# Kernel optimization log

Hardware: AMD Instinct MI355X
Metric: run time of the kernel (lower is better)

## Reference

```python
import jax, jax.numpy as jnp
import numpy as np

N = 50000      # nodes
E = 600000     # edges (before self loops)
F_IN = 128     # num_features
HID = 64       # num_hidden (per-head out channels of conv1)
HEADS = 8
NCLS = 16      # num_classes
NC = 16        # n_components (k_ricci feature dim)
NCP = 16       # n_components_p (e_poinc feature dim)


def _glorot(key, shape):
    lim = float(np.sqrt(6.0 / (shape[0] + shape[1])))
    return jax.random.uniform(key, shape, jnp.float32, -lim, lim)


def setup_inputs() -> dict:
    key = jax.random.key(0)
    ks = jax.random.split(key, 16)
    H1 = HEADS * HID  # 512
    return {
        "x": jax.random.normal(ks[0], (N, F_IN), jnp.float32),
        "edge_index": jax.random.randint(ks[1], (2, E), 0, N, jnp.int32),
        "alpha": jnp.ones((), jnp.float32),  # alpha_hp scalar
        "k_ricci": jax.random.normal(ks[2], (E + N, NC), jnp.float32),
        "e_poinc": jax.random.normal(ks[3], (N, NCP), jnp.float32),
        # conv1 params
        "W_src1": _glorot(ks[4], (F_IN, H1)),
        "h1_w1": _glorot(ks[5], (NC, HID)),
        "h1_w2": _glorot(ks[6], (HID, HID)),
        "h1_b2": jnp.zeros((HID,), jnp.float32),
        "p1_w1": _glorot(ks[7], (NCP, H1)),
        "p1_w2": _glorot(ks[8], (H1, H1)),
        "p1_b2": jnp.zeros((H1,), jnp.float32),
        "bias1": jnp.zeros((H1,), jnp.float32),
        # conv2 params (heads=1, concat=False)
        "W_src2": _glorot(ks[9], (H1, NCLS)),
        "h2_w1": _glorot(ks[10], (NC, NCLS)),
        "h2_w2": _glorot(ks[11], (NCLS, NCLS)),
        "h2_b2": jnp.zeros((NCLS,), jnp.float32),
        "p2_w1": _glorot(ks[12], (NCP, NCLS)),
        "p2_w2": _glorot(ks[13], (NCLS, NCLS)),
        "p2_b2": jnp.zeros((NCLS,), jnp.float32),
        "bias2": jnp.zeros((NCLS,), jnp.float32),
    }


def _segment_softmax(logits, seg, n):
    # PyG-style softmax over variable-sized segments, per channel.
    m = jax.ops.segment_max(logits, seg, num_segments=n)
    e = jnp.exp(logits - m[seg])
    s = jax.ops.segment_sum(e, seg, num_segments=n)
    return e / (s[seg] + 1e-16)


def _gat_layer(x, src, dst, k_ricci, e_poinc, alpha_hp,
               W_src, hw1, hw2, hb2, pw1, pw2, pb2, bias, H, C, concat):
    n = x.shape[0]
    xh = (x @ W_src).reshape(n, H, C)                                   # [N,H,C]
    # hmpnn MLP on per-edge Ricci features, then segment-softmax over SOURCE node
    edge_w = jax.nn.leaky_relu(k_ricci @ hw1, 0.2) @ hw2 + hb2          # [E',C]
    a = _segment_softmax(edge_w, src, n)                                # [E',C]
    msg = a[:, None, :] * xh[src]                                       # [E',H,C]
    agg = jax.ops.segment_sum(msg, dst, num_segments=n)                 # [N,H,C]
    out = agg.reshape(n, H * C) if concat else agg.mean(axis=1)
    out = out + bias
    # ham MLP on per-node Poincare features (+ extra leaky_relu, slope 0.01)
    p = jax.nn.leaky_relu(jax.nn.leaky_relu(e_poinc @ pw1, 0.2) @ pw2 + pb2, 0.01)
    return out + alpha_hp * p


def reference(x, edge_index, alpha, k_ricci, e_poinc,
              W_src1, h1_w1, h1_w2, h1_b2, p1_w1, p1_w2, p1_b2, bias1,
              W_src2, h2_w1, h2_w2, h2_b2, p2_w1, p2_w2, p2_b2, bias2):
    n = x.shape[0]
    loops = jnp.arange(n, dtype=edge_index.dtype)
    src = jnp.concatenate([edge_index[0], loops])   # add_self_loops
    dst = jnp.concatenate([edge_index[1], loops])
    h = _gat_layer(x, src, dst, k_ricci, e_poinc, alpha,
                   W_src1, h1_w1, h1_w2, h1_b2, p1_w1, p1_w2, p1_b2, bias1,
                   HEADS, HID, True)
    h = jax.nn.relu(h)
    o = _gat_layer(h, src, dst, k_ricci, e_poinc, alpha,
                   W_src2, h2_w1, h2_w2, h2_b2, p2_w1, p2_w2, p2_b2, bias2,
                   1, NCLS, False)
    return jax.nn.log_softmax(o, axis=1)
```

## Files before the change

kernel.cpp:

```cpp
#include <hip/hip_runtime.h>
#include <math.h>

#define N_NODES 50000
#define M_PAD   50048
#define N_EDGES 600000
#define E_TOT   650000
#define F_IN    128
#define HID     64
#define HEADS   8
#define H1      512
#define NCLS    16
#define NC      16
#define NCP     16
#define NBLK    ((N_NODES + 255) / 256)
#define FRNG    (N_NODES / 8)
#define FBPR    128
#define FPER    ((E_TOT + FBPR - 1) / FBPR)

typedef unsigned short u16;
typedef unsigned char  u8;
typedef __attribute__((ext_vector_type(8))) short short8;
typedef __attribute__((ext_vector_type(4))) float f32x4;
typedef __attribute__((ext_vector_type(2))) float f32x2;

__device__ __forceinline__ float bf2f(u16 h) {
    return __uint_as_float(((unsigned)h) << 16);
}
__device__ __forceinline__ u16 f2bf(float f) {
    unsigned u = __float_as_uint(f);
    u += 0x7fffu + ((u >> 16) & 1u);
    return (u16)(u >> 16);
}
__device__ __forceinline__ int edge_src(const int* __restrict__ ei, int e) {
    return (e < N_EDGES) ? ei[e] : (e - N_EDGES);
}
__device__ __forceinline__ int edge_dst(const int* __restrict__ ei, int e) {
    return (e < N_EDGES) ? ei[N_EDGES + e] : (e - N_EDGES);
}

__device__ __forceinline__ void gload16(const void* g, void* l) {
    __builtin_amdgcn_global_load_lds(
        (const __attribute__((address_space(1))) unsigned int*)g,
        (__attribute__((address_space(3))) unsigned int*)l, 16, 0, 0);
}

__global__ __launch_bounds__(256) void count_k(const int* __restrict__ ei,
                                               int* __restrict__ src_cnt, int* __restrict__ dst_cnt) {
    int e = blockIdx.x * 256 + threadIdx.x;
    if (e >= E_TOT) return;
    atomicAdd(&src_cnt[edge_src(ei, e)], 1);
    atomicAdd(&dst_cnt[edge_dst(ei, e)], 1);
}

__global__ __launch_bounds__(256) void scanA_k(const int* __restrict__ src_cnt,
                                               const int* __restrict__ dst_cnt,
                                               int* __restrict__ partials) {
    int pass = blockIdx.x >= NBLK;
    int b = blockIdx.x - pass * NBLK;
    const int* cnt = pass ? dst_cnt : src_cnt;
    int idx = b * 256 + threadIdx.x;
    int v = (idx < N_NODES) ? cnt[idx] : 0;
    __shared__ int red[4];
    #pragma unroll
    for (int off = 32; off; off >>= 1) v += __shfl_down(v, off, 64);
    if ((threadIdx.x & 63) == 0) red[threadIdx.x >> 6] = v;
    __syncthreads();
    if (threadIdx.x == 0) partials[blockIdx.x] = red[0] + red[1] + red[2] + red[3];
}

__global__ __launch_bounds__(512) void scanB_k(int* __restrict__ partials) {
    __shared__ int lds[512];
    int t = threadIdx.x;
    int seg = t >> 8, i = t & 255;
    int v = (i < NBLK) ? partials[seg * NBLK + i] : 0;
    lds[t] = v;
    __syncthreads();
    for (int d = 1; d < 256; d <<= 1) {
        int x = (i >= d) ? lds[seg * 256 + i - d] : 0;
        __syncthreads();
        lds[t] += x;
        __syncthreads();
    }
    if (i < NBLK) partials[seg * NBLK + i] = lds[t] - v;
}

__global__ __launch_bounds__(256) void scanC_k(const int* __restrict__ src_cnt,
                                               const int* __restrict__ dst_cnt,
                                               const int* __restrict__ partials,
                                               int* __restrict__ src_off, int* __restrict__ dst_off) {
    int pass = blockIdx.x >= NBLK;
    int b = blockIdx.x - pass * NBLK;
    const int* cnt = pass ? dst_cnt : src_cnt;
    int* off = pass ? dst_off : src_off;
    int base = partials[blockIdx.x];
    __shared__ int lds[256];
    int t = threadIdx.x;
    int idx = b * 256 + t;
    int v = (idx < N_NODES) ? cnt[idx] : 0;
    lds[t] = v;
    __syncthreads();
    for (int d = 1; d < 256; d <<= 1) {
        int x = (t >= d) ? lds[t - d] : 0;
        __syncthreads();
        lds[t] += x;
        __syncthreads();
    }
    if (idx < N_NODES) off[idx] = base + lds[t] - v;
    if (b == 0 && t == 0) off[N_NODES] = E_TOT;
}

__global__ __launch_bounds__(256) void fillD_k(const int* __restrict__ ei,
                                               const int* __restrict__ dst_off, int* __restrict__ dst_cur,
                                               int* __restrict__ deid, int* __restrict__ dsrc) {
    const int range = blockIdx.x & 7, slice = blockIdx.x >> 3;
    const int d0 = range * FRNG, d1 = d0 + FRNG;
    const int e0 = slice * FPER;
    const int e1 = (e0 + FPER < E_TOT) ? e0 + FPER : E_TOT;
    for (int e = e0 + threadIdx.x; e < e1; e += 256) {
        int d = edge_dst(ei, e);
        if (d < d0 || d >= d1) continue;
        int rd = dst_off[d] + atomicAdd(&dst_cur[d], 1);
        deid[rd] = e;
        dsrc[rd] = edge_src(ei, e);
    }
}

__global__ __launch_bounds__(256) void fillS_k(const int* __restrict__ dsrc,
                                               const int* __restrict__ src_off, int* __restrict__ src_cur,
                                               int* __restrict__ src_list) {
    const int range = blockIdx.x & 7, slice = blockIdx.x >> 3;
    const int s0 = range * FRNG, s1 = s0 + FRNG;
    const int r0 = slice * FPER;
    const int r1 = (r0 + FPER < E_TOT) ? r0 + FPER : E_TOT;
    for (int rd = r0 + threadIdx.x; rd < r1; rd += 256) {
        int s = dsrc[rd];
        if (s < s0 || s >= s1) continue;
        src_list[src_off[s] + atomicAdd(&src_cur[s], 1)] = rd;
    }
}

__global__ __launch_bounds__(256) void conv_a_k(const float* __restrict__ A, u16* __restrict__ Ap,
                                                int M, int Mp, int K) {
    int i = blockIdx.x * 256 + threadIdx.x;
    int total = (K >> 3) * Mp;
    if (i >= total) return;
    int r = i % Mp;
    int kb = i / Mp;
    u16* o = Ap + (size_t)i * 8;
    u16 tmp[8];
    if (r < M) {
        const float* a = A + (size_t)r * K + kb * 8;
        #pragma unroll
        for (int j = 0; j < 8; ++j) tmp[j] = f2bf(a[j]);
    } else {
        #pragma unroll
        for (int j = 0; j < 8; ++j) tmp[j] = 0;
    }
    *(ushort4*)o = *(ushort4*)tmp;
    *(ushort4*)(o + 4) = *(ushort4*)(tmp + 4);
}

__global__ __launch_bounds__(256) void conv_b_k(const float* __restrict__ B, u16* __restrict__ Bp,
                                                int K, int N) {
    int i = blockIdx.x * 256 + threadIdx.x;
    int total = (K >> 3) * N;
    if (i >= total) return;
    int n = i % N;
    int kb = i / N;
    u16 tmp[8];
    #pragma unroll
    for (int j = 0; j < 8; ++j) tmp[j] = f2bf(B[(size_t)(kb * 8 + j) * N + n]);
    u16* o = Bp + (size_t)i * 8;
    *(ushort4*)o = *(ushort4*)tmp;
    *(ushort4*)(o + 4) = *(ushort4*)(tmp + 4);
}

__device__ __forceinline__ void wfrag_one(const float* W, u16* o, int i, int K, int N) {
    int j = i & 7, lane = (i >> 3) & 63, rest = i >> 9;
    int nt = rest % (N / 16), ks = rest / (N / 16);
    int lm = lane & 15, quad = lane >> 4;
    int k = ks * 32 + quad * 8 + j, n = nt * 16 + lm;
    o[i] = (k < K) ? f2bf(W[(size_t)k * N + n]) : (u16)0;
}
__device__ __forceinline__ void wfrag_res(const float* W, u16* o, int i, int K, int N) {
    int j = i & 7, lane = (i >> 3) & 63, rest = i >> 9;
    int nt = rest % (N / 16), ks = rest / (N / 16);
    int lm = lane & 15, quad = lane >> 4;
    int k = ks * 32 + quad * 8 + j, n = nt * 16 + lm;
    float w = (k < K) ? W[(size_t)k * N + n] : 0.f;
    o[i] = f2bf(w - bf2f(f2bf(w)));
}
__global__ __launch_bounds__(256) void wfrag_all_k(
    const float* __restrict__ h1w1, const float* __restrict__ h1w2,
    const float* __restrict__ h2w1, const float* __restrict__ h2w2,
    const float* __restrict__ W2,
    u16* __restrict__ w1f, u16* __restrict__ w2f,
    u16* __restrict__ w3f, u16* __restrict__ w4f,
    u16* __restrict__ w2hf, u16* __restrict__ w2lf) {
    int i = blockIdx.x * 256 + threadIdx.x;
    if (i < 2048)       wfrag_one(h1w1, w1f, i, 16, 64);
    else if (i < 6144)  wfrag_one(h1w2, w2f, i - 2048, 64, 64);
    else if (i < 6656)  wfrag_one(h2w1, w3f, i - 6144, 16, 16);
    else if (i < 7168)  wfrag_one(h2w2, w4f, i - 6656, 16, 16);
    else if (i < 15360) wfrag_one(W2, w2hf, i - 7168, 512, 16);
    else if (i < 23552) wfrag_res(W2, w2lf, i - 15360, 512, 16);
}

template<int EPI>
__global__ __launch_bounds__(256) void mfma_gemm_k(
    const u16* __restrict__ Ap, const u16* __restrict__ Bp, u16* __restrict__ C,
    int M, int Mp, int Nn, int K,
    const float* __restrict__ bias, const u16* __restrict__ extra,
    const float* __restrict__ bias2, const float* __restrict__ alpha_p,
    const u16* __restrict__ w2hf, const u16* __restrict__ w2lf,
    float* __restrict__ xh2p)
{
    __shared__ __align__(16) char LSD[49152];
    const int t = threadIdx.x;
    const int wave = t >> 6, lane = t & 63;
    const int wm = (wave >> 1) * 64, wn = (wave & 1) * 64;
    const int lm = lane & 15, quad = lane >> 4;

    const int nwg = (int)(gridDim.y << 2);
    const int bid = (int)(blockIdx.y * 4 + blockIdx.x);
    const int qq = nwg >> 3, rr8 = nwg & 7;
    const int xcd = bid & 7, idx = bid >> 3;
    const int wg = (xcd < rr8 ? xcd * (qq + 1) : rr8 * (qq + 1) + (xcd - rr8) * qq) + idx;
    const int bn = (wg & 3) * 128;
    const int bm = (wg >> 2) * 128;

    const char* Ab = (const char*)Ap;
    const char* Bb = (const char*)Bp;

    f32x4 acc[4][4] = {};
    const int NT = K >> 5;

    auto stage = [&](int b, int ts) {
        const int kb0 = ts * 4;
        #pragma unroll
        for (int h = 0; h < 2; ++h) {
            const int ob = h * 4096 + wave * 1024;
            const int kb = kb0 + (ob >> 11);
            const int rem = (ob & 1024) + lane * 16;
            gload16(Ab + ((size_t)kb * Mp + bm) * 16 + rem, LSD + b * 8192 + ob);
            gload16(Bb + ((size_t)kb * Nn + bn) * 16 + rem, LSD + 24576 + b * 8192 + ob);
        }
    };
    auto compute = [&](int cb) {
        const u16* As = (const u16*)(LSD + cb * 8192);
        const u16* Bs = (const u16*)(LSD + 24576 + cb * 8192);
        short8 af[4], bfv[4];
        #pragma unroll
        for (int mi = 0; mi < 4; ++mi)
            af[mi] = *(const short8*)(As + quad * 1024 + (wm + mi * 16 + lm) * 8);
        #pragma unroll
        for (int nj = 0; nj < 4; ++nj)
            bfv[nj] = *(const short8*)(Bs + quad * 1024 + (wn + nj * 16 + lm) * 8);
        #pragma unroll
        for (int mi = 0; mi < 4; ++mi)
            #pragma unroll
            for (int nj = 0; nj < 4; ++nj)
                acc[mi][nj] = __builtin_amdgcn_mfma_f32_16x16x32_bf16(af[mi], bfv[nj], acc[mi][nj], 0, 0, 0);
    };

    stage(0, 0);
    stage(1, 1);
    #pragma unroll 1
    for (int ts = 0; ts < NT - 1; ++ts) {
        asm volatile("s_waitcnt vmcnt(4)" ::: "memory");
        __builtin_amdgcn_sched_barrier(0);
        __builtin_amdgcn_s_barrier();
        if (ts + 2 < NT) stage((ts + 2) % 3, ts + 2);
        compute(ts % 3);
    }
    asm volatile("s_waitcnt vmcnt(0)" ::: "memory");
    __builtin_amdgcn_sched_barrier(0);
    __builtin_amdgcn_s_barrier();
    compute((NT - 1) % 3);
    __syncthreads();

    float* Tf = (float*)LSD;
    const float alpha = (EPI == 0) ? 0.f : *alpha_p;
    short8 w2h[4], w2l[4];
    if (EPI != 0) {
        const int ksb = bn >> 5;
        #pragma unroll
        for (int kc = 0; kc < 4; ++kc) {
            w2h[kc] = *(const short8*)(w2hf + ((size_t)(ksb + kc) * 64 + lane) * 8);
            w2l[kc] = *(const short8*)(w2lf + ((size_t)(ksb + kc) * 64 + lane) * 8);
        }
    }
    #pragma unroll
    for (int pass = 0; pass < 2; ++pass) {
        if ((wave >> 1) == pass) {
            #pragma unroll
            for (int mi = 0; mi < 4; ++mi)
                #pragma unroll
                for (int r4 = 0; r4 < 4; ++r4) {
                    const int lr = mi * 16 + quad * 4 + r4;
                    const int sw = (lr & 7) << 2;
                    #pragma unroll
                    for (int nj = 0; nj < 4; ++nj)
                        Tf[lr * 128 + ((wn + nj * 16 + lm) ^ sw)] = acc[mi][nj][r4];
                }
        }
        __syncthreads();
        if (EPI == 0) {
            const int lrow = t & 63, chunk = t >> 6;
            const int col0 = chunk * 32;
            const int rr = bm + pass * 64 + lrow;
            if (rr < M) {
                const int sw = (lrow & 7) << 2;
                float v[32];
                #pragma unroll
                for (int j4 = 0; j4 < 8; ++j4) {
                    float4 f = *(const float4*)&Tf[lrow * 128 + ((col0 + j4 * 4) ^ sw)];
                    v[j4 * 4] = f.x; v[j4 * 4 + 1] = f.y; v[j4 * 4 + 2] = f.z; v[j4 * 4 + 3] = f.w;
                }
                const int gc0 = bn + col0;
                u16 pk[32];
                #pragma unroll
                for (int j = 0; j < 32; ++j) pk[j] = f2bf(v[j]);
                #pragma unroll
                for (int g = 0; g < 4; ++g)
                    *(short8*)(C + (size_t)rr * Nn + gc0 + g * 8) = *(const short8*)&pk[g * 8];
            }
        } else {
            u16* Hs = (u16*)(LSD + 32768);
            const int row = wave * 16 + lm;
            const int col0 = quad * 32;
            const int rr = bm + pass * 64 + row;
            const int gc0 = bn + col0;
            u16 hpk[32];
            if (rr < M) {
                const int sw = (row & 7) << 2;
                const u16* ex = extra + (size_t)rr * Nn + gc0;
                #pragma unroll
                for (int g = 0; g < 4; ++g) {
                    float4 f0 = *(const float4*)&Tf[row * 128 + ((col0 + g * 8) ^ sw)];
                    float4 f1 = *(const float4*)&Tf[row * 128 + ((col0 + g * 8 + 4) ^ sw)];
                    float vv8[8] = {f0.x, f0.y, f0.z, f0.w, f1.x, f1.y, f1.z, f1.w};
                    short8 e8 = *(const short8*)(ex + g * 8);
                    #pragma unroll
                    for (int j = 0; j < 8; ++j) {
                        const int cj = g * 8 + j;
                        float vv = vv8[j] + bias[gc0 + cj];
                        vv = vv > 0.f ? vv : 0.01f * vv;
                        float o = bf2f((u16)e8[j]) + bias2[gc0 + cj] + alpha * vv;
                        o = fmaxf(o, 0.f);
                        hpk[cj] = f2bf(o);
                    }
                }
            } else {
                #pragma unroll
                for (int j = 0; j < 32; ++j) hpk[j] = 0;
            }
            #pragma unroll
            for (int g = 0; g < 4; ++g) {
                const int ba = (row * 256 + quad * 64 + g * 16) ^ ((row & 7) << 4);
                *(short8*)((char*)Hs + ba) = *(const short8*)&hpk[g * 8];
            }
            __syncthreads();
            f32x4 axh = {};
            #pragma unroll
            for (int kc = 0; kc < 4; ++kc) {
                const int ba = (row * 256 + kc * 64 + quad * 16) ^ ((row & 7) << 4);
                short8 ha = *(const short8*)((const char*)Hs + ba);
                axh = __builtin_amdgcn_mfma_f32_16x16x32_bf16(ha, w2h[kc], axh, 0, 0, 0);
                axh = __builtin_amdgcn_mfma_f32_16x16x32_bf16(ha, w2l[kc], axh, 0, 0, 0);
            }
            #pragma unroll
            for (int r = 0; r < 4; ++r) {
                const int prow = bm + pass * 64 + wave * 16 + quad * 4 + r;
                if (prow < M)
                    xh2p[((size_t)(bn >> 7) * M_PAD + prow) * 16 + lm] = axh[r];
            }
        }
        __syncthreads();
    }
}

__global__ __launch_bounds__(256) void red4_k(const float* __restrict__ xh2p,
                                              float* __restrict__ xh2) {
    int i = blockIdx.x * 256 + threadIdx.x;
    if (i >= N_NODES * 4) return;
    const float4* P = (const float4*)xh2p;
    const size_t S = (size_t)M_PAD * 4;
    float4 a = P[i], b = P[S + i], c = P[2 * S + i], d = P[3 * S + i];
    float4 r;
    r.x = (a.x + b.x) + (c.x + d.x);
    r.y = (a.y + b.y) + (c.y + d.y);
    r.z = (a.z + b.z) + (c.z + d.z);
    r.w = (a.w + b.w) + (c.w + d.w);
    ((float4*)xh2)[i] = r;
}

__global__ __launch_bounds__(256) void gemm_t1_k(
    const float* __restrict__ ep, const float* __restrict__ W, u16* __restrict__ t1p)
{
    __shared__ float Bs[16][64];
    const int bm = blockIdx.y * 64, bn = blockIdx.x * 64;
    const int t = threadIdx.x;
    const int tx = t & 15, ty = t >> 4;
    *(float4*)&Bs[t >> 4][(t & 15) * 4] = *(const float4*)&W[(size_t)(t >> 4) * H1 + bn + (t & 15) * 4];
    __syncthreads();
    const int r0 = bm + ty * 4;
    const int c0 = bn + tx * 4;
    for (int i = 0; i < 4; ++i) {
        int r = r0 + i;
        if (r >= N_NODES) continue;
        float av[16];
        #pragma unroll
        for (int j4 = 0; j4 < 16; j4 += 4) {
            float4 v = *(const float4*)(ep + (size_t)r * NCP + j4);
            av[j4] = v.x; av[j4 + 1] = v.y; av[j4 + 2] = v.z; av[j4 + 3] = v.w;
        }
        u16 pk[4];
        #pragma unroll
        for (int q = 0; q < 4; ++q) {
            float s = 0.f;
            #pragma unroll
            for (int k = 0; k < 16; ++k) s = fmaf(av[k], Bs[k][tx * 4 + q], s);
            s = s > 0.f ? s : 0.2f * s;
            pk[q] = f2bf(s);
        }
        u16* o = t1p + ((size_t)(c0 >> 3) * M_PAD + r) * 8 + (c0 & 7);
        *(ushort4*)o = *(ushort4*)pk;
    }
}

#define TSTR 72
__global__ __launch_bounds__(256) void edge_mlps_k(
    const float* __restrict__ kr, const int* __restrict__ deid,
    const u16* __restrict__ w1f, const u16* __restrict__ w2f, const float* __restrict__ b2a,
    const u16* __restrict__ w3f, const u16* __restrict__ w4f, const float* __restrict__ b2b,
    u16* __restrict__ ebd, u16* __restrict__ ebd2)
{
    __shared__ __align__(16) u16 T[4][16 * TSTR];
    const int t = threadIdx.x, wv = t >> 6, lane = t & 63;
    const int lm = lane & 15, quad = lane >> 4;
    const int tile = blockIdx.x * 4 + wv;
    const int s0 = tile * 16;
    if (s0 >= E_TOT) return;
    u16* Tw = T[wv];

    short8 W1[4], W2[2][4];
    #pragma unroll
    for (int nt = 0; nt < 4; ++nt) W1[nt] = *(const short8*)(w1f + ((size_t)nt * 64 + lane) * 8);
    #pragma unroll
    for (int ks = 0; ks < 2; ++ks)
        #pragma unroll
        for (int nt = 0; nt < 4; ++nt)
            W2[ks][nt] = *(const short8*)(w2f + (((size_t)ks * 4 + nt) * 64 + lane) * 8);
    short8 W3 = *(const short8*)(w3f + (size_t)lane * 8);
    short8 W4 = *(const short8*)(w4f + (size_t)lane * 8);
    float b2av[4];
    #pragma unroll
    for (int nt = 0; nt < 4; ++nt) b2av[nt] = b2a[nt * 16 + lm];
    float b2bv = b2b[lm];

    const int e = deid[s0 + lm];
    short8 af = {};
    if (quad < 2) {
        const float* kp = kr + (size_t)e * NC + quad * 8;
        float4 v0 = *(const float4*)kp;
        float4 v1 = *(const float4*)(kp + 4);
        u16 tmp[8] = {f2bf(v0.x), f2bf(v0.y), f2bf(v0.z), f2bf(v0.w),
                      f2bf(v1.x), f2bf(v1.y), f2bf(v1.z), f2bf(v1.w)};
        af = *(const short8*)tmp;
    }

    f32x4 a1[4] = {};
    #pragma unroll
    for (int nt = 0; nt < 4; ++nt)
        a1[nt] = __builtin_amdgcn_mfma_f32_16x16x32_bf16(af, W1[nt], a1[nt], 0, 0, 0);
    #pragma unroll
    for (int nt = 0; nt < 4; ++nt)
        #pragma unroll
        for (int r = 0; r < 4; ++r) {
            float v = a1[nt][r];
            v = v > 0.f ? v : 0.2f * v;
            Tw[(quad * 4 + r) * TSTR + nt * 16 + lm] = f2bf(v);
        }
    __builtin_amdgcn_s_waitcnt(0);

    short8 a2[2];
    #pragma unroll
    for (int ks = 0; ks < 2; ++ks)
        a2[ks] = *(const short8*)&Tw[lm * TSTR + ks * 32 + quad * 8];
    f32x4 c2[4] = {};
    #pragma unroll
    for (int nt = 0; nt < 4; ++nt)
        #pragma unroll
        for (int ks = 0; ks < 2; ++ks)
            c2[nt] = __builtin_amdgcn_mfma_f32_16x16x32_bf16(a2[ks], W2[ks][nt], c2[nt], 0, 0, 0);
    #pragma unroll
    for (int nt = 0; nt < 4; ++nt)
        #pragma unroll
        for (int r = 0; r < 4; ++r)
            Tw[(quad * 4 + r) * TSTR + nt * 16 + lm] = f2bf(__expf(c2[nt][r] + b2av[nt]));
    __builtin_amdgcn_s_waitcnt(0);
    #pragma unroll
    for (int p = 0; p < 2; ++p) {
        int c = p * 64 + lane;
        int row = c >> 3, off = (c & 7) * 8;
        short8 v = *(const short8*)&Tw[row * TSTR + off];
        *(short8*)(ebd + (size_t)(s0 + row) * HID + off) = v;
    }

    f32x4 b1 = __builtin_amdgcn_mfma_f32_16x16x32_bf16(af, W3, (f32x4){}, 0, 0, 0);
    __builtin_amdgcn_s_waitcnt(0);
    #pragma unroll
    for (int r = 0; r < 4; ++r) {
        float v = b1[r];
        v = v > 0.f ? v : 0.2f * v;
        Tw[(quad * 4 + r) * TSTR + lm] = f2bf(v);
    }
    __builtin_amdgcn_s_waitcnt(0);
    short8 a3 = *(const short8*)&Tw[lm * TSTR + quad * 8];
    f32x4 c3 = __builtin_amdgcn_mfma_f32_16x16x32_bf16(a3, W4, (f32x4){}, 0, 0, 0);
    #pragma unroll
    for (int r = 0; r < 4; ++r)
        Tw[(quad * 4 + r) * TSTR + lm] = f2bf(__expf(c3[r] + b2bv));
    __builtin_amdgcn_s_waitcnt(0);
    if (lane < 32) {
        int row = lane >> 1, off = (lane & 1) * 8;
        short8 v = *(const short8*)&Tw[row * TSTR + off];
        *(short8*)(ebd2 + (size_t)(s0 + row) * NCLS + off) = v;
    }
}

__global__ __launch_bounds__(256) void s1inv_k(
    const u16* __restrict__ ebd, const int* __restrict__ src_off, const int* __restrict__ src_list,
    u16* __restrict__ xb)
{
    __shared__ float sinv[4][64];
    int gid = blockIdx.x * 256 + threadIdx.x;
    int wid = gid >> 6, lane = gid & 63, wv = threadIdx.x >> 6;
    if (wid >= N_NODES) return;
    int o0 = src_off[wid], o1 = src_off[wid + 1];
    float s0 = 0.f, s1 = 0.f, s2 = 0.f, s3 = 0.f;
    int i = o0;
    for (; i + 3 < o1; i += 4) {
        int l0 = src_list[i], l1 = src_list[i + 1], l2 = src_list[i + 2], l3 = src_list[i + 3];
        s0 += bf2f(ebd[(size_t)l0 * HID + lane]);
        s1 += bf2f(ebd[(size_t)l1 * HID + lane]);
        s2 += bf2f(ebd[(size_t)l2 * HID + lane]);
        s3 += bf2f(ebd[(size_t)l3 * HID + lane]);
    }
    for (; i < o1; ++i) {
        int sl = src_list[i];
        s0 += bf2f(ebd[(size_t)sl * HID + lane]);
    }
    sinv[wv][lane] = 1.f / (((s0 + s1) + (s2 + s3)) + 1e-16f);
    __builtin_amdgcn_s_waitcnt(0);

    const u16* xr = xb + (size_t)wid * H1 + lane * 8;
    short8 x8 = *(const short8*)xr;
    float y[8];
    #pragma unroll
    for (int j = 0; j < 8; ++j)
        y[j] = bf2f((u16)x8[j]) * sinv[wv][(lane * 8 + j) & 63];
    int p0 = 0, p1 = 0;
    p0 = __builtin_amdgcn_cvt_pk_fp8_f32(y[0], y[1], p0, false);
    p0 = __builtin_amdgcn_cvt_pk_fp8_f32(y[2], y[3], p0, true);
    p1 = __builtin_amdgcn_cvt_pk_fp8_f32(y[4], y[5], p1, false);
    p1 = __builtin_amdgcn_cvt_pk_fp8_f32(y[6], y[7], p1, true);
    uint2 pk; pk.x = (unsigned)p0; pk.y = (unsigned)p1;
    *(uint2*)((u8*)xb + (size_t)wid * (H1 * 2) + lane * 8) = pk;
}

__global__ __launch_bounds__(256) void msg1_k(
    const u16* __restrict__ ebd, const u8* __restrict__ xq,
    const int* __restrict__ dsrc, const int* __restrict__ dst_off,
    u16* __restrict__ aggb)
{
    int gid = blockIdx.x * 256 + threadIdx.x;
    int wid = gid >> 6, lane = gid & 63;
    if (wid >= N_NODES) return;
    int o0 = dst_off[wid], o1 = dst_off[wid + 1];
    const int a_off = (lane & 7) * 8;
    float acc[8] = {};
    int i = o0;
    for (; i + 3 < o1; i += 4) {
        int s0 = __builtin_nontemporal_load(dsrc + i);
        int s1 = __builtin_nontemporal_load(dsrc + i + 1);
        int s2 = __builtin_nontemporal_load(dsrc + i + 2);
        int s3 = __builtin_nontemporal_load(dsrc + i + 3);
        short8 a0 = __builtin_nontemporal_load((const short8*)(ebd + (size_t)i * HID + a_off));
        short8 a1 = __builtin_nontemporal_load((const short8*)(ebd + (size_t)(i + 1) * HID + a_off));
        short8 a2 = __builtin_nontemporal_load((const short8*)(ebd + (size_t)(i + 2) * HID + a_off));
        short8 a3 = __builtin_nontemporal_load((const short8*)(ebd + (size_t)(i + 3) * HID + a_off));
        uint2 q0 = *(const uint2*)(xq + (size_t)s0 * 1024 + lane * 8);
        uint2 q1 = *(const uint2*)(xq + (size_t)s1 * 1024 + lane * 8);
        uint2 q2 = *(const uint2*)(xq + (size_t)s2 * 1024 + lane * 8);
        uint2 q3 = *(const uint2*)(xq + (size_t)s3 * 1024 + lane * 8);
        const uint2 qs[4] = {q0, q1, q2, q3};
        const short8 as[4] = {a0, a1, a2, a3};
        #pragma unroll
        for (int u = 0; u < 4; ++u) {
            f32x2 d0 = __builtin_amdgcn_cvt_pk_f32_fp8((int)qs[u].x, false);
            f32x2 d1 = __builtin_amdgcn_cvt_pk_f32_fp8((int)qs[u].x, true);
            f32x2 d2 = __builtin_amdgcn_cvt_pk_f32_fp8((int)qs[u].y, false);
            f32x2 d3 = __builtin_amdgcn_cvt_pk_f32_fp8((int)qs[u].y, true);
            float xv[8] = {d0.x, d0.y, d1.x, d1.y, d2.x, d2.y, d3.x, d3.y};
            #pragma unroll
            for (int j = 0; j < 8; ++j)
                acc[j] = fmaf(bf2f((u16)as[u][j]), xv[j], acc[j]);
        }
    }
    for (; i < o1; ++i) {
        int s = __builtin_nontemporal_load(dsrc + i);
        short8 a8 = __builtin_nontemporal_load((const short8*)(ebd + (size_t)i * HID + a_off));
        uint2 q = *(const uint2*)(xq + (size_t)s * 1024 + lane * 8);
        f32x2 d0 = __builtin_amdgcn_cvt_pk_f32_fp8((int)q.x, false);
        f32x2 d1 = __builtin_amdgcn_cvt_pk_f32_fp8((int)q.x, true);
        f32x2 d2 = __builtin_amdgcn_cvt_pk_f32_fp8((int)q.y, false);
        f32x2 d3 = __builtin_amdgcn_cvt_pk_f32_fp8((int)q.y, true);
        float xv[8] = {d0.x, d0.y, d1.x, d1.y, d2.x, d2.y, d3.x, d3.y};
        #pragma unroll
        for (int j = 0; j < 8; ++j)
            acc[j] = fmaf(bf2f((u16)a8[j]), xv[j], acc[j]);
    }
    u16 pk[8];
    #pragma unroll
    for (int j = 0; j < 8; ++j) pk[j] = f2bf(acc[j]);
    __builtin_nontemporal_store(*(const short8*)pk, (short8*)(aggb + (size_t)wid * H1 + lane * 8));
}

__global__ __launch_bounds__(256) void s2sum_k(
    const u16* __restrict__ ebd2, const int* __restrict__ src_off, const int* __restrict__ src_list,
    float* __restrict__ inv2)
{
    int t = threadIdx.x;
    int g = blockIdx.x * 16 + (t >> 4), c = t & 15;
    if (g >= N_NODES) return;
    int o0 = src_off[g], o1 = src_off[g + 1];
    float sum = 0.f;
    for (int i = o0; i < o1; ++i) {
        int sl = src_list[i];
        sum += bf2f(ebd2[(size_t)sl * NCLS + c]);
    }
    inv2[(size_t)g * NCLS + c] = 1.f / (sum + 1e-16f);
}

__global__ __launch_bounds__(256) void msg2_k(
    const u16* __restrict__ ebd2, const float* __restrict__ inv2,
    const float* __restrict__ xh2, const int* __restrict__ dsrc,
    const int* __restrict__ dst_off, float* __restrict__ agg2)
{
    int t = threadIdx.x;
    int g = blockIdx.x * 16 + (t >> 4), c = t & 15;
    if (g >= N_NODES) return;
    int o0 = dst_off[g], o1 = dst_off[g + 1];
    float acc = 0.f;
    for (int i = o0; i < o1; ++i) {
        int s = dsrc[i];
        float a = bf2f(ebd2[(size_t)i * NCLS + c]) * inv2[(size_t)s * NCLS + c];
        acc = fmaf(a, xh2[(size_t)s * NCLS + c], acc);
    }
    agg2[(size_t)g * NCLS + c] = acc;
}

__global__ __launch_bounds__(256) void final_k(
    const float* __restrict__ agg2, const float* __restrict__ ep,
    const float* __restrict__ pw1, const float* __restrict__ pw2,
    const float* __restrict__ pb2, const float* __restrict__ bias,
    const float* __restrict__ alpha_p, float* __restrict__ out)
{
    __shared__ float s1w[256], s2w[256], sb[16], sbias[16];
    const int t = threadIdx.x;
    s1w[t] = pw1[t];
    s2w[t] = pw2[t];
    if (t < 16) { sb[t] = pb2[t]; sbias[t] = bias[t]; }
    __syncthreads();
    const int v = blockIdx.x * 256 + t;
    if (v >= N_NODES) return;
    float alpha = *alpha_p;
    float e_[16];
    #pragma unroll
    for (int j4 = 0; j4 < 16; j4 += 4) {
        float4 vv = *(const float4*)(ep + (size_t)v * 16 + j4);
        e_[j4] = vv.x; e_[j4 + 1] = vv.y; e_[j4 + 2] = vv.z; e_[j4 + 3] = vv.w;
    }
    float t2[16];
    #pragma unroll
    for (int c = 0; c < 16; ++c) {
        float s = 0.f;
        #pragma unroll
        for (int j = 0; j < 16; ++j) s = fmaf(e_[j], s1w[j * 16 + c], s);
        t2[c] = s > 0.f ? s : 0.2f * s;
    }
    float o[16];
    #pragma unroll
    for (int c4 = 0; c4 < 16; c4 += 4) {
        float4 ag = *(const float4*)(agg2 + (size_t)v * 16 + c4);
        float agv[4] = {ag.x, ag.y, ag.z, ag.w};
        #pragma unroll
        for (int q = 0; q < 4; ++q) {
            int c = c4 + q;
            float p = sb[c];
            #pragma unroll
            for (int j = 0; j < 16; ++j) p = fmaf(t2[j], s2w[j * 16 + c], p);
            p = p > 0.f ? p : 0.01f * p;
            o[c] = agv[q] + sbias[c] + alpha * p;
        }
    }
    float mx = o[0];
    #pragma unroll
    for (int c = 1; c < 16; ++c) mx = fmaxf(mx, o[c]);
    float se = 0.f;
    #pragma unroll
    for (int c = 0; c < 16; ++c) se += expf(o[c] - mx);
    float lse = mx + logf(se);
    #pragma unroll
    for (int c4 = 0; c4 < 16; c4 += 4)
        *(float4*)(out + (size_t)v * 16 + c4) =
            make_float4(o[c4] - lse, o[c4 + 1] - lse, o[c4 + 2] - lse, o[c4 + 3] - lse);
}

extern "C" void kernel_launch(void* const* d_in, const int* in_sizes, int n_in,
                              void* d_out, int out_size, void* d_ws, size_t ws_size,
                              hipStream_t stream) {
    const float* x    = (const float*)d_in[0];
    const int*   ei   = (const int*)d_in[1];
    const float* alpha= (const float*)d_in[2];
    const float* kr   = (const float*)d_in[3];
    const float* ep   = (const float*)d_in[4];
    const float* W1   = (const float*)d_in[5];
    const float* h1w1 = (const float*)d_in[6];
    const float* h1w2 = (const float*)d_in[7];
    const float* h1b2 = (const float*)d_in[8];
    const float* p1w1 = (const float*)d_in[9];
    const float* p1w2 = (const float*)d_in[10];
    const float* p1b2 = (const float*)d_in[11];
    const float* b1   = (const float*)d_in[12];
    const float* W2   = (const float*)d_in[13];
    const float* h2w1 = (const float*)d_in[14];
    const float* h2w2 = (const float*)d_in[15];
    const float* h2b2 = (const float*)d_in[16];
    const float* p2w1 = (const float*)d_in[17];
    const float* p2w2 = (const float*)d_in[18];
    const float* p2b2 = (const float*)d_in[19];
    const float* b2   = (const float*)d_in[20];
    float* out = (float*)d_out;

    char* p = (char*)d_ws;
    auto alloc = [&](size_t bytes) { char* r = p; p += (bytes + 255) & ~(size_t)255; return r; };

    char* r0    = alloc((size_t)64 * M_PAD * 16);
    u16*  xb    = (u16*)r0;
    u16*  t1p   = (u16*)r0;
    u16*  aggb  = (u16*)alloc((size_t)N_NODES * H1 * 2);
    char* ebr   = alloc((size_t)E_TOT * HID * 2);
    u16*  ebd   = (u16*)ebr;
    u16*  ebd2  = (u16*)alloc((size_t)E_TOT * NCLS * 2);
    char* xpr   = alloc((size_t)16 * M_PAD * 16);
    u16*  xp    = (u16*)xpr;
    float* xh2p = (float*)xpr;
    u16*  W1p   = (u16*)alloc((size_t)16 * H1 * 16);
    u16*  p1w2p = (u16*)alloc((size_t)64 * H1 * 16);
    u16*  w1f   = (u16*)alloc(2048 * 2);
    u16*  w2f   = (u16*)alloc(4096 * 2);
    u16*  w3f   = (u16*)alloc(512 * 2);
    u16*  w4f   = (u16*)alloc(512 * 2);
    u16*  w2hf  = (u16*)alloc(8192 * 2);
    u16*  w2lf  = (u16*)alloc(8192 * 2);
    int* src_cnt  = (int*)alloc(N_NODES * 4);
    int* dst_cnt  = (int*)alloc(N_NODES * 4);
    int* src_cur  = (int*)alloc(N_NODES * 4);
    int* dst_cur  = (int*)alloc(N_NODES * 4);
    int* partials = (int*)alloc(2 * NBLK * 4);
    int* src_off  = (int*)alloc((N_NODES + 1) * 4);
    int* dst_off  = (int*)alloc((N_NODES + 1) * 4);
    int* src_list = (int*)alloc((size_t)E_TOT * 4);
    int* deid     = (int*)alloc((size_t)E_TOT * 4);
    int* dsrc     = (int*)alloc((size_t)E_TOT * 4);
    float* xh2  = (float*)alloc((size_t)N_NODES * NCLS * 4);
    float* agg2 = (float*)alloc((size_t)N_NODES * NCLS * 4);
    float* inv2 = (float*)alloc((size_t)N_NODES * NCLS * 4);

    const dim3 blk(256);
    const int EB = (E_TOT + 255) / 256;
    const int WB = (N_NODES * 64 + 255) / 256;
    const int GB16 = (N_NODES + 15) / 16;
    const dim3 gmm(512 / 128, M_PAD / 128);
    const int MLPB = (E_TOT / 16 + 3) / 4;

    hipMemsetAsync(src_cnt, 0, (char*)partials - (char*)src_cnt, stream);
    count_k<<<EB, blk, 0, stream>>>(ei, src_cnt, dst_cnt);
    scanA_k<<<2 * NBLK, blk, 0, stream>>>(src_cnt, dst_cnt, partials);
    scanB_k<<<1, 512, 0, stream>>>(partials);
    scanC_k<<<2 * NBLK, blk, 0, stream>>>(src_cnt, dst_cnt, partials, src_off, dst_off);
    fillD_k<<<8 * FBPR, blk, 0, stream>>>(ei, dst_off, dst_cur, deid, dsrc);
    fillS_k<<<8 * FBPR, blk, 0, stream>>>(dsrc, src_off, src_cur, src_list);
    conv_a_k<<<(16 * M_PAD + 255) / 256, blk, 0, stream>>>(x, xp, N_NODES, M_PAD, F_IN);
    conv_b_k<<<(16 * H1 + 255) / 256, blk, 0, stream>>>(W1, W1p, F_IN, H1);
    conv_b_k<<<(64 * H1 + 255) / 256, blk, 0, stream>>>(p1w2, p1w2p, H1, H1);
    wfrag_all_k<<<92, blk, 0, stream>>>(h1w1, h1w2, h2w1, h2w2, W2,
                                        w1f, w2f, w3f, w4f, w2hf, w2lf);

    mfma_gemm_k<0><<<gmm, blk, 0, stream>>>(xp, W1p, xb, N_NODES, M_PAD, H1, F_IN,
                                            nullptr, nullptr, nullptr, nullptr,
                                            nullptr, nullptr, nullptr);
    edge_mlps_k<<<MLPB, blk, 0, stream>>>(kr, deid, w1f, w2f, h1b2, w3f, w4f, h2b2, ebd, ebd2);
    s1inv_k<<<WB, blk, 0, stream>>>(ebd, src_off, src_list, xb);
    msg1_k<<<WB, blk, 0, stream>>>(ebd, (const u8*)xb, dsrc, dst_off, aggb);
    gemm_t1_k<<<dim3(8, (N_NODES + 63) / 64), blk, 0, stream>>>(ep, p1w1, t1p);
    mfma_gemm_k<3><<<gmm, blk, 0, stream>>>(t1p, p1w2p, nullptr, N_NODES, M_PAD, H1, H1,
                                            p1b2, aggb, b1, alpha, w2hf, w2lf, xh2p);
    red4_k<<<(N_NODES * 4 + 255) / 256, blk, 0, stream>>>(xh2p, xh2);

    s2sum_k<<<GB16, blk, 0, stream>>>(ebd2, src_off, src_list, inv2);
    msg2_k<<<GB16, blk, 0, stream>>>(ebd2, inv2, xh2, dsrc, dst_off, agg2);
    final_k<<<(N_NODES + 255) / 256, blk, 0, stream>>>(agg2, ep, p2w1, p2w2, p2b2, b2, alpha, out);
}
```

Before: 628.3 us.

## Load GEMM B fragments directly to registers and shrink LDS for occupancy

The MFMA GEMM no longer stages B tiles through shared memory. Each wave loads its B fragments straight from global into double-buffered registers, and the main loop is unrolled by two to alternate the buffers. This cuts LDS from 48KB to 32KB, launch bounds ask for 4 blocks per SM, and the epilogue reuses the freed LDS for the H tile, adding an extra barrier. The W2 epilogue fragments are now loaded inside the loop instead of being held in registers, which trades register pressure for redundant global loads.

New measurement: 617.8 us. No clear change (-1.7%).

```diff
diff --git a/kernel.cpp b/kernel.cpp
--- a/kernel.cpp
+++ b/kernel.cpp
@@ -207,7 +207,7 @@
 }
 
 template<int EPI>
-__global__ __launch_bounds__(256) void mfma_gemm_k(
+__global__ __launch_bounds__(256, 4) void mfma_gemm_k(
     const u16* __restrict__ Ap, const u16* __restrict__ Bp, u16* __restrict__ C,
     int M, int Mp, int Nn, int K,
     const float* __restrict__ bias, const u16* __restrict__ extra,
@@ -215,7 +215,7 @@
     const u16* __restrict__ w2hf, const u16* __restrict__ w2lf,
     float* __restrict__ xh2p)
 {
-    __shared__ __align__(16) char LSD[49152];
+    __shared__ __align__(16) char LSD[32768];
     const int t = threadIdx.x;
     const int wave = t >> 6, lane = t & 63;
     const int wm = (wave >> 1) * 64, wn = (wave & 1) * 64;
@@ -230,12 +230,14 @@
     const int bm = (wg >> 2) * 128;
 
     const char* Ab = (const char*)Ap;
-    const char* Bb = (const char*)Bp;
+    size_t cbase[4];
+    #pragma unroll
+    for (int nj = 0; nj < 4; ++nj) cbase[nj] = (size_t)(bn + wn + nj * 16 + lm) * 8;
 
     f32x4 acc[4][4] = {};
     const int NT = K >> 5;
 
-    auto stage = [&](int b, int ts) {
+    auto stageA = [&](int b, int ts) {
         const int kb0 = ts * 4;
         #pragma unroll
         for (int h = 0; h < 2; ++h) {
@@ -243,53 +245,58 @@
             const int kb = kb0 + (ob >> 11);
             const int rem = (ob & 1024) + lane * 16;
             gload16(Ab + ((size_t)kb * Mp + bm) * 16 + rem, LSD + b * 8192 + ob);
-            gload16(Bb + ((size_t)kb * Nn + bn) * 16 + rem, LSD + 24576 + b * 8192 + ob);
         }
     };
-    auto compute = [&](int cb) {
+    auto loadB = [&](short8 (&bf)[4], int ts) {
+        const u16* Bq = Bp + (size_t)(ts * 4 + quad) * Nn * 8;
+        #pragma unroll
+        for (int nj = 0; nj < 4; ++nj) bf[nj] = *(const short8*)(Bq + cbase[nj]);
+    };
+    auto compute = [&](int cb, short8 (&bf)[4]) {
         const u16* As = (const u16*)(LSD + cb * 8192);
-        const u16* Bs = (const u16*)(LSD + 24576 + cb * 8192);
-        short8 af[4], bfv[4];
+        short8 af[4];
         #pragma unroll
         for (int mi = 0; mi < 4; ++mi)
             af[mi] = *(const short8*)(As + quad * 1024 + (wm + mi * 16 + lm) * 8);
-        #pragma unroll
-        for (int nj = 0; nj < 4; ++nj)
-            bfv[nj] = *(const short8*)(Bs + quad * 1024 + (wn + nj * 16 + lm) * 8);
         #pragma unroll
         for (int mi = 0; mi < 4; ++mi)
             #pragma unroll
             for (int nj = 0; nj < 4; ++nj)
-                acc[mi][nj] = __builtin_amdgcn_mfma_f32_16x16x32_bf16(af[mi], bfv[nj], acc[mi][nj], 0, 0, 0);
+                acc[mi][nj] = __builtin_amdgcn_mfma_f32_16x16x32_bf16(af[mi], bf[nj], acc[mi][nj], 0, 0, 0);
     };
 
-    stage(0, 0);
-    stage(1, 1);
+    short8 b0[4], b1[4];
+    stageA(0, 0);
+    loadB(b0, 0);
+    stageA(1, 1);
     #pragma unroll 1
-    for (int ts = 0; ts < NT - 1; ++ts) {
-        asm volatile("s_waitcnt vmcnt(4)" ::: "memory");
+    for (int ts = 0; ts < NT - 2; ts += 2) {
+        asm volatile("s_waitcnt vmcnt(6)" ::: "memory");
         __builtin_amdgcn_sched_barrier(0);
         __builtin_amdgcn_s_barrier();
-        if (ts + 2 < NT) stage((ts + 2) % 3, ts + 2);
-        compute(ts % 3);
-    }
-    asm volatile("s_waitcnt vmcnt(0)" ::: "memory");
+        loadB(b1, ts + 1);
+        stageA((ts + 2) % 3, ts + 2);
+        compute(ts % 3, b0);
+        asm volatile("s_waitcnt vmcnt(6)" ::: "memory");
+        __builtin_amdgcn_sched_barrier(0);
+        __builtin_amdgcn_s_barrier();
+        loadB(b0, ts + 2);
+        stageA((ts + 3) % 3, ts + 3);
+        compute((ts + 1) % 3, b1);
+    }
+    asm volatile("s_waitcnt vmcnt(6)" ::: "memory");
     __builtin_amdgcn_sched_barrier(0);
     __builtin_amdgcn_s_barrier();
-    compute((NT - 1) % 3);
+    loadB(b1, NT - 1);
+    compute((NT - 2) % 3, b0);
+    asm volatile("s_waitcnt vmcnt(4)" ::: "memory");
+    __builtin_amdgcn_sched_barrier(0);
+    __builtin_amdgcn_s_barrier();
+    compute((NT - 1) % 3, b1);
     __syncthreads();
 
     float* Tf = (float*)LSD;
     const float alpha = (EPI == 0) ? 0.f : *alpha_p;
-    short8 w2h[4], w2l[4];
-    if (EPI != 0) {
-        const int ksb = bn >> 5;
-        #pragma unroll
-        for (int kc = 0; kc < 4; ++kc) {
-            w2h[kc] = *(const short8*)(w2hf + ((size_t)(ksb + kc) * 64 + lane) * 8);
-            w2l[kc] = *(const short8*)(w2lf + ((size_t)(ksb + kc) * 64 + lane) * 8);
-        }
-    }
     #pragma unroll
     for (int pass = 0; pass < 2; ++pass) {
         if ((wave >> 1) == pass) {
@@ -326,7 +333,7 @@
                     *(short8*)(C + (size_t)rr * Nn + gc0 + g * 8) = *(const short8*)&pk[g * 8];
             }
         } else {
-            u16* Hs = (u16*)(LSD + 32768);
+            u16* Hs = (u16*)LSD;
             const int row = wave * 16 + lm;
             const int col0 = quad * 32;
             const int rr = bm + pass * 64 + row;
@@ -355,6 +362,7 @@
                 #pragma unroll
                 for (int j = 0; j < 32; ++j) hpk[j] = 0;
             }
+            __syncthreads();
             #pragma unroll
             for (int g = 0; g < 4; ++g) {
                 const int ba = (row * 256 + quad * 64 + g * 16) ^ ((row & 7) << 4);
@@ -362,12 +370,15 @@
             }
             __syncthreads();
             f32x4 axh = {};
+            const int ksb = bn >> 5;
             #pragma unroll
             for (int kc = 0; kc < 4; ++kc) {
                 const int ba = (row * 256 + kc * 64 + quad * 16) ^ ((row & 7) << 4);
                 short8 ha = *(const short8*)((const char*)Hs + ba);
-                axh = __builtin_amdgcn_mfma_f32_16x16x32_bf16(ha, w2h[kc], axh, 0, 0, 0);
-                axh = __builtin_amdgcn_mfma_f32_16x16x32_bf16(ha, w2l[kc], axh, 0, 0, 0);
+                short8 wh = *(const short8*)(w2hf + ((size_t)(ksb + kc) * 64 + lane) * 8);
+                short8 wl = *(const short8*)(w2lf + ((size_t)(ksb + kc) * 64 + lane) * 8);
+                axh = __builtin_amdgcn_mfma_f32_16x16x32_bf16(ha, wh, axh, 0, 0, 0);
+                axh = __builtin_amdgcn_mfma_f32_16x16x32_bf16(ha, wl, axh, 0, 0, 0);
             }
             #pragma unroll
             for (int r = 0; r < 4; ++r) {
```
